# Kernel tuning notes

Measured on AMD Instinct MI355X. Metric: run time of the kernel, lower is better.

Reference implementation:

```python
import jax, jax.numpy as jnp
import numpy as np

B, S, E, H, FFN, NQ = 4, 2048, 1024, 16, 4096, 8
DK = E // H
EPS = 1e-5


def setup_inputs() -> dict:
    key = jax.random.key(0)
    ks = jax.random.split(key, 8)
    x = jax.random.normal(ks[0], (B, S, E), dtype=jnp.float32)
    theta = jax.random.normal(ks[1], (NQ,), dtype=jnp.float32)  # RY angles
    w1 = jax.random.normal(ks[2], (FFN, NQ), dtype=jnp.float32) / np.sqrt(NQ)
    b1 = jnp.zeros((FFN,), dtype=jnp.float32)
    w2 = jax.random.normal(ks[3], (E, FFN), dtype=jnp.float32) / np.sqrt(FFN)
    b2 = jnp.zeros((E,), dtype=jnp.float32)
    gamma1 = jnp.ones((E,), dtype=jnp.float32)
    beta1 = jnp.zeros((E,), dtype=jnp.float32)
    gamma2 = jnp.ones((E,), dtype=jnp.float32)
    beta2 = jnp.zeros((E,), dtype=jnp.float32)
    return {"x": x, "theta": theta, "w1": w1, "b1": b1, "w2": w2, "b2": b2,
            "gamma1": gamma1, "beta1": beta1, "gamma2": gamma2, "beta2": beta2}


def _layernorm(h, g, b):
    mu = jnp.mean(h, axis=-1, keepdims=True)
    var = jnp.mean(jnp.square(h - mu), axis=-1, keepdims=True)
    return (h - mu) * jax.lax.rsqrt(var + EPS) * g + b


def _attention(x):
    # q = k = v = separate_heads(x); no projection weights in the original.
    q = x.reshape(B, S, H, DK).transpose(0, 2, 1, 3)  # [B,H,S,DK]
    scores = jnp.einsum("bhqd,bhkd->bhqk", q, q) / np.sqrt(DK)
    probs = jax.nn.softmax(scores, axis=-1)
    out = jnp.einsum("bhqk,bhkd->bhqd", probs, q)
    return out.transpose(0, 2, 1, 3).reshape(B, S, E)


def _ffn_quantum(h, theta, w1, b1, w2, b2):
    # Per-token circuit: RX(x_i) then RY(theta_i) on independent qubits,
    # measure PauliZ -> <Z_i> = cos(x_i) * cos(theta_i). Batched over all tokens.
    qout = jnp.cos(h[..., :NQ]) * jnp.cos(theta)  # [B,S,NQ]
    hid = jax.nn.relu(jnp.einsum("bsq,fq->bsf", qout, w1) + b1)
    return jnp.einsum("bsf,ef->bse", hid, w2) + b2


def reference(x, theta, w1, b1, w2, b2, gamma1, beta1, gamma2, beta2):
    attn_out = _attention(x)
    h = _layernorm(x + attn_out, gamma1, beta1)
    ffn_out = _ffn_quantum(h, theta, w1, b1, w2, b2)
    return _layernorm(h + ffn_out, gamma2, beta2)
```

## Files before the change

kernel.cpp:

```cpp
#include <hip/hip_runtime.h>


#define Bq 4
#define Sq 2048
#define Eq 1024
#define Hq 16
#define DKq 64
#define FFNq 4096
#define NQq 8
#define LOG2E 1.44269504f

typedef unsigned int u32;
typedef unsigned short u16;
typedef _Float16 f16;
typedef f16 f16x8 __attribute__((ext_vector_type(8)));
typedef __fp16 fp16x2 __attribute__((ext_vector_type(2)));
typedef float f32x4 __attribute__((ext_vector_type(4)));

#if __has_builtin(__builtin_amdgcn_exp2f)
#define EXP2F __builtin_amdgcn_exp2f
#else
#define EXP2F exp2f
#endif

#define MFMA(a, b, c) __builtin_amdgcn_mfma_f32_16x16x32_f16((a), (b), (c), 0, 0, 0)

#define GLL(g, l)                                                          \
  __builtin_amdgcn_global_load_lds(                                        \
      (const __attribute__((address_space(1))) u32*)(g),                   \
      (__attribute__((address_space(3))) u32*)(l), 16, 0, 0)

__device__ __forceinline__ u16 f2h(float x) {
  f16 t = (f16)x;
  return __builtin_bit_cast(u16, t);
}
__device__ __forceinline__ float h2f(u16 w) {
  return (float)__builtin_bit_cast(f16, w);
}
#if __has_builtin(__builtin_amdgcn_cvt_pkrtz)
__device__ __forceinline__ u32 pkrtz(float a, float b) {
  fp16x2 r = __builtin_amdgcn_cvt_pkrtz(a, b);
  return __builtin_bit_cast(u32, r);
}
#else
__device__ __forceinline__ u32 pkrtz(float a, float b) {
  return (u32)f2h(a) | ((u32)f2h(b) << 16);
}
#endif

union F8 { f16x8 v; u32 w[4]; u16 h[8]; f16 e[8]; };

__global__ void k_prep(const float* __restrict__ x, u16* __restrict__ xh,
                       u16* __restrict__ xt, const float* __restrict__ w2src,
                       uint4* __restrict__ w2dst) {
  __shared__ u16 tile[64 * 72];
  const int tid = threadIdx.x;
  const int bx = blockIdx.x;
  if (bx >= 2048) {
    const int i = (bx - 2048) * 256 + tid;
    const int n8 = (Eq * FFNq) / 8;
    if (i < n8) {
      const float4* s = (const float4*)w2src + 2 * (long)i;
      float4 a = s[0], b = s[1];
      uint4 r;
      r.x = pkrtz(a.x, a.y);
      r.y = pkrtz(a.z, a.w);
      r.z = pkrtz(b.x, b.y);
      r.w = pkrtz(b.z, b.w);
      w2dst[i] = r;
    }
    return;
  }
  const int sb = bx & 31, bh = bx >> 5;
  const int b = bh >> 4, h = bh & 15;
  const int s0 = sb * 64;
  const int r = tid >> 2, cq = tid & 3;
  const float* xp = x + ((long)(b * Sq + s0 + r)) * Eq + h * 64 + cq * 16;
  float4 f0 = ((const float4*)xp)[0], f1 = ((const float4*)xp)[1];
  float4 f2 = ((const float4*)xp)[2], f3 = ((const float4*)xp)[3];
  u32 w[8];
  w[0] = pkrtz(f0.x, f0.y); w[1] = pkrtz(f0.z, f0.w);
  w[2] = pkrtz(f1.x, f1.y); w[3] = pkrtz(f1.z, f1.w);
  w[4] = pkrtz(f2.x, f2.y); w[5] = pkrtz(f2.z, f2.w);
  w[6] = pkrtz(f3.x, f3.y); w[7] = pkrtz(f3.z, f3.w);
  uint4* xo = (uint4*)(xh + ((long)(b * Sq + s0 + r)) * Eq + h * 64 + cq * 16);
  xo[0] = make_uint4(w[0], w[1], w[2], w[3]);
  xo[1] = make_uint4(w[4], w[5], w[6], w[7]);
  uint4* tp = (uint4*)(tile + r * 72 + cq * 16);
  tp[0] = make_uint4(w[0], w[1], w[2], w[3]);
  tp[1] = make_uint4(w[4], w[5], w[6], w[7]);
  __syncthreads();
  const int d = tid >> 2, rq = tid & 3;
  u32 o[8];
#pragma unroll
  for (int i = 0; i < 8; ++i) {
    u32 lo = tile[(rq * 16 + 2 * i) * 72 + d];
    u32 hi = tile[(rq * 16 + 2 * i + 1) * 72 + d];
    o[i] = lo | (hi << 16);
  }
  uint4* to = (uint4*)(xt + ((long)(bh * 64 + d)) * Sq + s0 + rq * 16);
  to[0] = make_uint4(o[0], o[1], o[2], o[3]);
  to[1] = make_uint4(o[4], o[5], o[6], o[7]);
}

__global__ __launch_bounds__(512, 4) void k_attn(const u16* __restrict__ xh,
                                                 const u16* __restrict__ xt,
                                                 u16* __restrict__ attn) {
  __shared__ __align__(16) u16 lds[34816];
  u16* Pl = lds + 16384;

  const int tid = threadIdx.x;
  const int wave = tid >> 6, lane = tid & 63;
  const int n = lane & 15, quad = lane >> 4;

  const int bx = blockIdx.x;
  const int qb = bx >> 6, bh = bx & 63;
  const int b = bh >> 4, h = bh & 15;

  const u16* xh_bh = xh + (long)b * Sq * Eq + h * 64;
  const u16* xt_bh = xt + (long)bh * 64 * Sq;

  const float SC = 0.125f * LOG2E;
  F8 qf[2][2];
  float shift[2], lrow[2] = {0.f, 0.f};
#pragma unroll
  for (int nt = 0; nt < 2; ++nt) {
    const int q = qb * 256 + wave * 32 + nt * 16 + n;
    const u16* qp = xh_bh + (long)q * Eq + quad * 8;
    F8 a, c;
    a.v = *(const f16x8*)qp;
    c.v = *(const f16x8*)(qp + 32);
    float s2 = 0.f;
#pragma unroll
    for (int i = 0; i < 8; ++i) {
      float va = (float)a.e[i], vc = (float)c.e[i];
      s2 += va * va + vc * vc;
      qf[nt][0].e[i] = a.e[i] * (f16)SC;
      qf[nt][1].e[i] = c.e[i] * (f16)SC;
    }
    s2 += __shfl_xor(s2, 16);
    s2 += __shfl_xor(s2, 32);
    shift[nt] = SC * s2;
  }

  const int r8 = lane >> 3;
  const int cl = (lane & 7) ^ r8;
  const u16* gK = xh_bh + (long)(wave * 8 + r8) * Eq + cl * 8;
  const u16* gV = xt_bh + (long)(wave * 8 + r8) * Sq + cl * 8;
  const int lK = wave * 512;
  const int lV = 4096 + wave * 512;

  u16* cur = lds;
  u16* nxt = lds + 8192;

  GLL(gK, cur + lK);
  GLL(gV, cur + lV);
  gK += 64 * Eq;
  gV += 64;

  f32x4 O[2][4] = {};
  u16* Pw = Pl + wave * 2304;

  for (int kb = 0; kb < Sq / 64; ++kb) {
    __syncthreads();
    if (kb < Sq / 64 - 1) {
      GLL(gK, nxt + lK);
      GLL(gV, nxt + lV);
      gK += 64 * Eq;
      gV += 64;
    }
    u16* Kl = cur;
    u16* Vt = cur + 4096;

    f32x4 ST[2][4];
#pragma unroll
    for (int nt = 0; nt < 2; ++nt) {
      const float ms = -shift[nt];
#pragma unroll
      for (int mt = 0; mt < 4; ++mt) {
        ST[nt][mt][0] = ms; ST[nt][mt][1] = ms;
        ST[nt][mt][2] = ms; ST[nt][mt][3] = ms;
      }
    }
    __builtin_amdgcn_s_setprio(1);
#pragma unroll
    for (int mt = 0; mt < 4; ++mt) {
#pragma unroll
      for (int c = 0; c < 2; ++c) {
        f16x8 af = *(const f16x8*)(Kl + (mt * 16 + n) * 64 +
                                   (((c * 4 + quad) ^ (n & 7)) * 8));
#pragma unroll
        for (int nt = 0; nt < 2; ++nt)
          ST[nt][mt] = MFMA(af, qf[nt][c].v, ST[nt][mt]);
      }
    }
    __builtin_amdgcn_s_setprio(0);

#pragma unroll
    for (int nt = 0; nt < 2; ++nt) {
      float ls = 0.f;
#pragma unroll
      for (int mt = 0; mt < 4; ++mt) {
        float p0 = EXP2F(ST[nt][mt][0]);
        float p1 = EXP2F(ST[nt][mt][1]);
        float p2 = EXP2F(ST[nt][mt][2]);
        float p3 = EXP2F(ST[nt][mt][3]);
        ls += (p0 + p1) + (p2 + p3);
        const int ch = 2 * mt + (quad >> 1);
        *(uint2*)(Pw + nt * 1152 + n * 72 + ch * 8 + (quad & 1) * 4) =
            make_uint2(pkrtz(p0, p1), pkrtz(p2, p3));
      }
      lrow[nt] += ls;
    }

    __builtin_amdgcn_s_setprio(1);
#pragma unroll
    for (int c = 0; c < 2; ++c) {
      const int pc = (c * 4 + quad) * 8;
      f16x8 pf[2];
#pragma unroll
      for (int nt = 0; nt < 2; ++nt)
        pf[nt] = *(const f16x8*)(Pw + nt * 1152 + n * 72 + pc);
      const int vc = ((c * 4 + quad) ^ (n & 7)) * 8;
#pragma unroll
      for (int dt = 0; dt < 4; ++dt) {
        f16x8 vf = *(const f16x8*)(Vt + (dt * 16 + n) * 64 + vc);
#pragma unroll
        for (int nt = 0; nt < 2; ++nt) O[nt][dt] = MFMA(vf, pf[nt], O[nt][dt]);
      }
    }
    __builtin_amdgcn_s_setprio(0);
    u16* t = cur; cur = nxt; nxt = t;
  }

#pragma unroll
  for (int nt = 0; nt < 2; ++nt) {
    float l = lrow[nt];
    l += __shfl_xor(l, 16);
    l += __shfl_xor(l, 32);
    const float inv = 1.0f / l;
    const int q = qb * 256 + wave * 32 + nt * 16 + n;
    u16* op = attn + (long)b * Sq * Eq + (long)q * Eq + h * 64;
#pragma unroll
    for (int dt = 0; dt < 4; ++dt) {
      u32 w0 = pkrtz(O[nt][dt][0] * inv, O[nt][dt][1] * inv);
      u32 w1 = pkrtz(O[nt][dt][2] * inv, O[nt][dt][3] * inv);
      *(uint2*)(op + dt * 16 + quad * 4) = make_uint2(w0, w1);
    }
  }
}

__global__ void k_ln1(const u16* __restrict__ xh, const u16* __restrict__ attn,
                      const float* __restrict__ g, const float* __restrict__ be,
                      const float* __restrict__ theta, u16* __restrict__ hout,
                      u16* __restrict__ qout) {
  const long t = blockIdx.x;
  const int tid = threadIdx.x;
  uint2 xw = ((const uint2*)(xh + t * Eq))[tid];
  uint2 aw = ((const uint2*)(attn + t * Eq))[tid];
  float v0 = h2f(xw.x & 0xffff) + h2f(aw.x & 0xffff);
  float v1 = h2f(xw.x >> 16) + h2f(aw.x >> 16);
  float v2 = h2f(xw.y & 0xffff) + h2f(aw.y & 0xffff);
  float v3 = h2f(xw.y >> 16) + h2f(aw.y >> 16);
  float s = (v0 + v1) + (v2 + v3);
  float s2 = v0 * v0 + v1 * v1 + v2 * v2 + v3 * v3;
#pragma unroll
  for (int o = 1; o < 64; o <<= 1) {
    s += __shfl_xor(s, o);
    s2 += __shfl_xor(s2, o);
  }
  __shared__ float red[8];
  const int wv = tid >> 6, ln = tid & 63;
  if (ln == 0) { red[wv] = s; red[4 + wv] = s2; }
  __syncthreads();
  s = red[0] + red[1] + red[2] + red[3];
  s2 = red[4] + red[5] + red[6] + red[7];
  const float mu = s * (1.f / Eq);
  const float var = s2 * (1.f / Eq) - mu * mu;
  const float rstd = rsqrtf(var + 1e-5f);
  float4 gv = ((const float4*)g)[tid];
  float4 bv = ((const float4*)be)[tid];
  float o0 = (v0 - mu) * rstd * gv.x + bv.x;
  float o1 = (v1 - mu) * rstd * gv.y + bv.y;
  float o2 = (v2 - mu) * rstd * gv.z + bv.z;
  float o3 = (v3 - mu) * rstd * gv.w + bv.w;
  ((uint2*)(hout + t * Eq))[tid] = make_uint2(pkrtz(o0, o1), pkrtz(o2, o3));
  if (tid < 2) {
    float hv[4] = {o0, o1, o2, o3};
    float q[4];
#pragma unroll
    for (int i = 0; i < 4; ++i) q[i] = cosf(hv[i]) * cosf(theta[tid * 4 + i]);
    *(uint2*)(qout + t * NQq + tid * 4) = make_uint2(pkrtz(q[0], q[1]), pkrtz(q[2], q[3]));
  }
}

__global__ void k_hid(const u16* __restrict__ qout, const float* __restrict__ w1,
                      const float* __restrict__ b1, u16* __restrict__ hid) {
  __shared__ float qs[256][8];
  const int tid = threadIdx.x;
  const int fb = blockIdx.x & 63, tb = blockIdx.x >> 6;
  const int f0 = fb * 64, t0 = tb * 256;
  {
    uint4 qw = *(const uint4*)(qout + (long)(t0 + tid) * NQq);
    qs[tid][0] = h2f(qw.x & 0xffff); qs[tid][1] = h2f(qw.x >> 16);
    qs[tid][2] = h2f(qw.y & 0xffff); qs[tid][3] = h2f(qw.y >> 16);
    qs[tid][4] = h2f(qw.z & 0xffff); qs[tid][5] = h2f(qw.z >> 16);
    qs[tid][6] = h2f(qw.w & 0xffff); qs[tid][7] = h2f(qw.w >> 16);
  }
  __syncthreads();
  const int wave = tid >> 6, lane = tid & 63;
  const int f = f0 + lane;
  const float4* wp = (const float4*)(w1 + (long)f * NQq);
  float4 wa = wp[0], wb = wp[1];
  const float bb = b1[f];
  const int trow = wave * 64;
  u16* op = hid + (long)(t0 + trow) * FFNq + f;
#pragma unroll 4
  for (int i = 0; i < 64; ++i) {
    const float* q = qs[trow + i];
    float acc = bb + q[0] * wa.x + q[1] * wa.y + q[2] * wa.z + q[3] * wa.w +
                q[4] * wb.x + q[5] * wb.y + q[6] * wb.z + q[7] * wb.w;
    acc = fmaxf(acc, 0.f);
    op[(long)i * FFNq] = f2h(acc);
  }
}

__global__ __launch_bounds__(512, 4) void k_gemm(const u16* __restrict__ Ah,
                                                 const u16* __restrict__ Bh,
                                                 u16* __restrict__ C) {
  __shared__ __align__(16) u16 lds[32768];
  const int tid = threadIdx.x;
  const int wave = tid >> 6, lane = tid & 63;
  const int n = lane & 15, quad = lane >> 4;
  const int wm = wave >> 2, wn = wave & 3;
  const int bid = blockIdx.x;
  const int m0 = ((bid & 7) * 8 + (bid >> 6)) * 128;
  const int n0 = ((bid >> 3) & 7) * 128;
  const int r8 = lane >> 3;
  const int cl = (lane & 7) ^ r8;

  const u16* gA0 = Ah + (long)(m0 + wave * 16 + r8) * FFNq + cl * 8;
  const u16* gA1 = gA0 + 8 * FFNq;
  const u16* gB0 = Bh + (long)(n0 + wave * 16 + r8) * FFNq + cl * 8;
  const u16* gB1 = gB0 + 8 * FFNq;
  const int lA0 = (wave * 16) * 64, lA1 = lA0 + 512;
  const int lB0 = 8192 + (wave * 16) * 64, lB1 = lB0 + 512;

  u16* cur = lds;
  u16* nxt = lds + 16384;

  GLL(gA0, cur + lA0); GLL(gA1, cur + lA1);
  GLL(gB0, cur + lB0); GLL(gB1, cur + lB1);
  gA0 += 64; gA1 += 64; gB0 += 64; gB1 += 64;

  f32x4 acc[4][2] = {};
  for (int it = 0; it < FFNq / 64; ++it) {
    __syncthreads();
    if (it < FFNq / 64 - 1) {
      GLL(gA0, nxt + lA0); GLL(gA1, nxt + lA1);
      GLL(gB0, nxt + lB0); GLL(gB1, nxt + lB1);
      gA0 += 64; gA1 += 64; gB0 += 64; gB1 += 64;
    }
    u16* La = cur;
    u16* Lb = cur + 8192;
#pragma unroll
    for (int c = 0; c < 2; ++c) {
      const int sw = ((c * 4 + quad) ^ (n & 7)) * 8;
      f16x8 af[4], bf[2];
#pragma unroll
      for (int i = 0; i < 4; ++i)
        af[i] = *(const f16x8*)(La + (wm * 64 + i * 16 + n) * 64 + sw);
#pragma unroll
      for (int j = 0; j < 2; ++j)
        bf[j] = *(const f16x8*)(Lb + (wn * 32 + j * 16 + n) * 64 + sw);
#pragma unroll
      for (int i = 0; i < 4; ++i)
#pragma unroll
        for (int j = 0; j < 2; ++j) acc[i][j] = MFMA(af[i], bf[j], acc[i][j]);
    }
    u16* t = cur; cur = nxt; nxt = t;
  }
#pragma unroll
  for (int i = 0; i < 4; ++i) {
    const int row = m0 + wm * 64 + i * 16 + quad * 4;
#pragma unroll
    for (int j = 0; j < 2; ++j) {
      u16* cp = C + (long)row * Eq + n0 + wn * 32 + j * 16 + n;
      cp[0] = f2h(acc[i][j][0]);
      cp[Eq] = f2h(acc[i][j][1]);
      cp[2 * Eq] = f2h(acc[i][j][2]);
      cp[3 * Eq] = f2h(acc[i][j][3]);
    }
  }
}

__global__ void k_ln2(const u16* __restrict__ hin, const u16* __restrict__ ffn,
                      const float* __restrict__ b2, const float* __restrict__ g,
                      const float* __restrict__ be, float* __restrict__ out) {
  const long t = blockIdx.x;
  const int tid = threadIdx.x;
  uint2 hw = ((const uint2*)(hin + t * Eq))[tid];
  uint2 fw = ((const uint2*)(ffn + t * Eq))[tid];
  float4 b2v = ((const float4*)b2)[tid];
  float v0 = h2f(hw.x & 0xffff) + h2f(fw.x & 0xffff) + b2v.x;
  float v1 = h2f(hw.x >> 16) + h2f(fw.x >> 16) + b2v.y;
  float v2 = h2f(hw.y & 0xffff) + h2f(fw.y & 0xffff) + b2v.z;
  float v3 = h2f(hw.y >> 16) + h2f(fw.y >> 16) + b2v.w;
  float s = (v0 + v1) + (v2 + v3);
  float s2 = v0 * v0 + v1 * v1 + v2 * v2 + v3 * v3;
#pragma unroll
  for (int o = 1; o < 64; o <<= 1) {
    s += __shfl_xor(s, o);
    s2 += __shfl_xor(s2, o);
  }
  __shared__ float red[8];
  const int wv = tid >> 6, ln = tid & 63;
  if (ln == 0) { red[wv] = s; red[4 + wv] = s2; }
  __syncthreads();
  s = red[0] + red[1] + red[2] + red[3];
  s2 = red[4] + red[5] + red[6] + red[7];
  const float mu = s * (1.f / Eq);
  const float var = s2 * (1.f / Eq) - mu * mu;
  const float rstd = rsqrtf(var + 1e-5f);
  float4 gv = ((const float4*)g)[tid];
  float4 bv = ((const float4*)be)[tid];
  float4 o;
  o.x = (v0 - mu) * rstd * gv.x + bv.x;
  o.y = (v1 - mu) * rstd * gv.y + bv.y;
  o.z = (v2 - mu) * rstd * gv.z + bv.z;
  o.w = (v3 - mu) * rstd * gv.w + bv.w;
  ((float4*)(out + t * Eq))[tid] = o;
}

extern "C" void kernel_launch(void* const* d_in, const int* in_sizes, int n_in,
                              void* d_out, int out_size, void* d_ws, size_t ws_size,
                              hipStream_t stream) {
  const float* x = (const float*)d_in[0];
  const float* theta = (const float*)d_in[1];
  const float* w1 = (const float*)d_in[2];
  const float* b1 = (const float*)d_in[3];
  const float* w2 = (const float*)d_in[4];
  const float* b2 = (const float*)d_in[5];
  const float* g1 = (const float*)d_in[6];
  const float* be1 = (const float*)d_in[7];
  const float* g2 = (const float*)d_in[8];
  const float* be2 = (const float*)d_in[9];
  float* out = (float*)d_out;

  char* ws = (char*)d_ws;
  u16* attn = (u16*)(ws);
  u16* h = (u16*)(ws + 16777216);
  u16* xh = (u16*)(ws + 33554432);
  u16* xt = (u16*)(ws + 50331648);
  u16* ffn = (u16*)(ws + 67108864);
  u16* hid = (u16*)(ws + 83886080);
  u16* w2h = (u16*)(ws + 150994944);
  u16* qout = (u16*)(ws + 159383552);

  k_prep<<<2 * Bq * Hq * (Sq / 64), 256, 0, stream>>>(x, xh, xt, w2, (uint4*)w2h);
  k_attn<<<Bq * Hq * (Sq / 256), 512, 0, stream>>>(xh, xt, attn);
  k_ln1<<<Bq * Sq, 256, 0, stream>>>(xh, attn, g1, be1, theta, h, qout);
  k_hid<<<(Bq * Sq / 256) * (FFNq / 64), 256, 0, stream>>>(qout, w1, b1, hid);
  k_gemm<<<(Bq * Sq / 128) * (Eq / 128), 512, 0, stream>>>(hid, w2h, ffn);
  k_ln2<<<Bq * Sq, 256, 0, stream>>>(h, ffn, b2, g2, be2, out);
}
```

Measured before the change: 289.3 us.

## Restructure FFN GEMM into 256x128 tiles with triple-buffered interleaved pipeline

The second FFN GEMM moves from 128x128 to 256x128 block tiles, so each wave now computes a 64x64 output. The K loop becomes a three-stage LDS ring with global-to-LDS loads split into chunks and interleaved with MFMA phases. Those phases are separated by barriers and raised wave priority (setprio) around the MFMA bursts. The aim is more data reuse per LDS load and better hiding of global load latency, at the cost of 144KB LDS per block, one block per CU, and half as many blocks.

```diff
diff --git a/kernel.cpp b/kernel.cpp
--- a/kernel.cpp
+++ b/kernel.cpp
@@ -29,6 +29,13 @@
   __builtin_amdgcn_global_load_lds(                                        \
       (const __attribute__((address_space(1))) u32*)(g),                   \
       (__attribute__((address_space(3))) u32*)(l), 16, 0, 0)
+
+#define BARRIER()                         \
+  do {                                    \
+    asm volatile("" ::: "memory");        \
+    __builtin_amdgcn_s_barrier();         \
+    asm volatile("" ::: "memory");        \
+  } while (0)
 
 __device__ __forceinline__ u16 f2h(float x) {
   f16 t = (f16)x;
@@ -325,67 +332,126 @@
   }
 }
 
-__global__ __launch_bounds__(512, 4) void k_gemm(const u16* __restrict__ Ah,
+__global__ __launch_bounds__(512, 1) void k_gemm(const u16* __restrict__ Ah,
                                                  const u16* __restrict__ Bh,
                                                  u16* __restrict__ C) {
-  __shared__ __align__(16) u16 lds[32768];
+  __shared__ __align__(16) u16 lds[73728];
   const int tid = threadIdx.x;
   const int wave = tid >> 6, lane = tid & 63;
   const int n = lane & 15, quad = lane >> 4;
-  const int wm = wave >> 2, wn = wave & 3;
+  const int wm = wave >> 1, wn = wave & 1;
   const int bid = blockIdx.x;
-  const int m0 = ((bid & 7) * 8 + (bid >> 6)) * 128;
+  const int m0 = ((bid & 7) * 4 + (bid >> 6)) * 256;
   const int n0 = ((bid >> 3) & 7) * 128;
   const int r8 = lane >> 3;
   const int cl = (lane & 7) ^ r8;
 
-  const u16* gA0 = Ah + (long)(m0 + wave * 16 + r8) * FFNq + cl * 8;
-  const u16* gA1 = gA0 + 8 * FFNq;
-  const u16* gB0 = Bh + (long)(n0 + wave * 16 + r8) * FFNq + cl * 8;
-  const u16* gB1 = gB0 + 8 * FFNq;
-  const int lA0 = (wave * 16) * 64, lA1 = lA0 + 512;
-  const int lB0 = 8192 + (wave * 16) * 64, lB1 = lB0 + 512;
-
-  u16* cur = lds;
-  u16* nxt = lds + 16384;
-
-  GLL(gA0, cur + lA0); GLL(gA1, cur + lA1);
-  GLL(gB0, cur + lB0); GLL(gB1, cur + lB1);
-  gA0 += 64; gA1 += 64; gB0 += 64; gB1 += 64;
-
-  f32x4 acc[4][2] = {};
-  for (int it = 0; it < FFNq / 64; ++it) {
-    __syncthreads();
-    if (it < FFNq / 64 - 1) {
-      GLL(gA0, nxt + lA0); GLL(gA1, nxt + lA1);
-      GLL(gB0, nxt + lB0); GLL(gB1, nxt + lB1);
-      gA0 += 64; gA1 += 64; gB0 += 64; gB1 += 64;
-    }
-    u16* La = cur;
-    u16* Lb = cur + 8192;
-#pragma unroll
-    for (int c = 0; c < 2; ++c) {
-      const int sw = ((c * 4 + quad) ^ (n & 7)) * 8;
-      f16x8 af[4], bf[2];
-#pragma unroll
-      for (int i = 0; i < 4; ++i)
-        af[i] = *(const f16x8*)(La + (wm * 64 + i * 16 + n) * 64 + sw);
-#pragma unroll
-      for (int j = 0; j < 2; ++j)
-        bf[j] = *(const f16x8*)(Lb + (wn * 32 + j * 16 + n) * 64 + sw);
-#pragma unroll
-      for (int i = 0; i < 4; ++i)
-#pragma unroll
-        for (int j = 0; j < 2; ++j) acc[i][j] = MFMA(af[i], bf[j], acc[i][j]);
-    }
-    u16* t = cur; cur = nxt; nxt = t;
-  }
+  const u16* gA[4];
+  const u16* gB[2];
+  int lA[4], lB[2];
+#pragma unroll
+  for (int j = 0; j < 4; ++j) {
+    gA[j] = Ah + (long)(m0 + j * 64 + wave * 8 + r8) * FFNq + cl * 8;
+    lA[j] = (j * 64 + wave * 8) * 64;
+  }
+#pragma unroll
+  for (int j = 0; j < 2; ++j) {
+    gB[j] = Bh + (long)(n0 + j * 64 + wave * 8 + r8) * FFNq + cl * 8;
+    lB[j] = 16384 + (j * 64 + wave * 8) * 64;
+  }
+
+  auto stageA = [&](int j, u16* base) { GLL(gA[j], base + lA[j]); gA[j] += 64; };
+  auto stageB = [&](int j, u16* base) { GLL(gB[j], base + lB[j]); gB[j] += 64; };
+  auto stageTile = [&](u16* base) {
+    stageA(0, base); stageA(1, base); stageA(2, base); stageA(3, base);
+    stageB(0, base); stageB(1, base);
+  };
+
+  stageTile(lds);
+  stageTile(lds + 24576);
+  asm volatile("s_waitcnt vmcnt(6)" ::: "memory");
+  BARRIER();
+
+  f32x4 acc[4][4] = {};
+  const int arow = wm * 64 + n;
+  const int brow = wn * 64 + n;
+
+  for (int t = 0; t < FFNq / 64; ++t) {
+    u16* La = lds + (t % 3) * 24576;
+    u16* Lb = La + 16384;
+    u16* Sn = lds + ((t + 2) % 3) * 24576;
+    const bool pre = (t < FFNq / 64 - 2);
+    const int sw0 = (quad ^ (n & 7)) * 8;
+    const int sw1 = ((4 + quad) ^ (n & 7)) * 8;
+
+    f16x8 af0, af1, af2, af3, bf[4];
+
+    if (pre) { stageA(0, Sn); stageA(1, Sn); }
+    af0 = *(const f16x8*)(La + (arow + 0) * 64 + sw0);
+    af1 = *(const f16x8*)(La + (arow + 16) * 64 + sw0);
+#pragma unroll
+    for (int j = 0; j < 4; ++j)
+      bf[j] = *(const f16x8*)(Lb + (brow + j * 16) * 64 + sw0);
+    BARRIER();
+    __builtin_amdgcn_s_setprio(1);
+#pragma unroll
+    for (int j = 0; j < 4; ++j) acc[0][j] = MFMA(af0, bf[j], acc[0][j]);
+#pragma unroll
+    for (int j = 0; j < 4; ++j) acc[1][j] = MFMA(af1, bf[j], acc[1][j]);
+    __builtin_amdgcn_s_setprio(0);
+    BARRIER();
+
+    if (pre) { stageA(2, Sn); stageA(3, Sn); }
+    af2 = *(const f16x8*)(La + (arow + 32) * 64 + sw0);
+    af3 = *(const f16x8*)(La + (arow + 48) * 64 + sw0);
+    BARRIER();
+    __builtin_amdgcn_s_setprio(1);
+#pragma unroll
+    for (int j = 0; j < 4; ++j) acc[2][j] = MFMA(af2, bf[j], acc[2][j]);
+#pragma unroll
+    for (int j = 0; j < 4; ++j) acc[3][j] = MFMA(af3, bf[j], acc[3][j]);
+    __builtin_amdgcn_s_setprio(0);
+    BARRIER();
+
+    if (pre) stageB(0, Sn);
+    af0 = *(const f16x8*)(La + (arow + 0) * 64 + sw1);
+    af1 = *(const f16x8*)(La + (arow + 16) * 64 + sw1);
+#pragma unroll
+    for (int j = 0; j < 4; ++j)
+      bf[j] = *(const f16x8*)(Lb + (brow + j * 16) * 64 + sw1);
+    BARRIER();
+    __builtin_amdgcn_s_setprio(1);
+#pragma unroll
+    for (int j = 0; j < 4; ++j) acc[0][j] = MFMA(af0, bf[j], acc[0][j]);
+#pragma unroll
+    for (int j = 0; j < 4; ++j) acc[1][j] = MFMA(af1, bf[j], acc[1][j]);
+    __builtin_amdgcn_s_setprio(0);
+    BARRIER();
+
+    if (pre) stageB(1, Sn);
+    af2 = *(const f16x8*)(La + (arow + 32) * 64 + sw1);
+    af3 = *(const f16x8*)(La + (arow + 48) * 64 + sw1);
+    if (pre) {
+      asm volatile("s_waitcnt vmcnt(6)" ::: "memory");
+    } else {
+      asm volatile("s_waitcnt vmcnt(0)" ::: "memory");
+    }
+    BARRIER();
+    __builtin_amdgcn_s_setprio(1);
+#pragma unroll
+    for (int j = 0; j < 4; ++j) acc[2][j] = MFMA(af2, bf[j], acc[2][j]);
+#pragma unroll
+    for (int j = 0; j < 4; ++j) acc[3][j] = MFMA(af3, bf[j], acc[3][j]);
+    __builtin_amdgcn_s_setprio(0);
+    BARRIER();
+  }
+
 #pragma unroll
   for (int i = 0; i < 4; ++i) {
     const int row = m0 + wm * 64 + i * 16 + quad * 4;
 #pragma unroll
-    for (int j = 0; j < 2; ++j) {
-      u16* cp = C + (long)row * Eq + n0 + wn * 32 + j * 16 + n;
+    for (int j = 0; j < 4; ++j) {
+      u16* cp = C + (long)row * Eq + n0 + wn * 64 + j * 16 + n;
       cp[0] = f2h(acc[i][j][0]);
       cp[Eq] = f2h(acc[i][j][1]);
       cp[2 * Eq] = f2h(acc[i][j][2]);
@@ -461,6 +527,6 @@
   k_attn<<<Bq * Hq * (Sq / 256), 512, 0, stream>>>(xh, xt, attn);
   k_ln1<<<Bq * Sq, 256, 0, stream>>>(xh, attn, g1, be1, theta, h, qout);
   k_hid<<<(Bq * Sq / 256) * (FFNq / 64), 256, 0, stream>>>(qout, w1, b1, hid);
-  k_gemm<<<(Bq * Sq / 128) * (Eq / 128), 512, 0, stream>>>(hid, w2h, ffn);
+  k_gemm<<<(Bq * Sq / 256) * (Eq / 128), 512, 0, stream>>>(hid, w2h, ffn);
   k_ln2<<<Bq * Sq, 256, 0, stream>>>(h, ffn, b2, g2, be2, out);
 }
```

Result: slower. 298.8 us (+3.3%).
